# Performance work log

Hardware: AMD Instinct MI355X
Metric: run time of the kernel (lower is better)

Reference implementation:

```python
import jax, jax.numpy as jnp
import numpy as np

B, T, H = 32, 8192, 128

def setup_inputs() -> dict:
    key = jax.random.key(0)
    k1, k2, k3, k4, k5, k6 = jax.random.split(key, 6)
    stdv = 1.0 / np.sqrt(H)
    return {
        "hidden": jax.random.normal(k1, (B, H), jnp.float32),
        "encoder_outputs": jax.random.normal(k2, (T, B, H), jnp.float32),
        "len_seq": jax.random.randint(k3, (B,), 1, T + 1),  # valid lengths in [1, T]
        "W_attn": jax.random.normal(k4, (H, 2 * H), jnp.float32) * stdv,
        "b_attn": jnp.zeros((H,), jnp.float32),
        "v": jax.random.uniform(k5, (H,), jnp.float32, -stdv, stdv),
    }

def reference(hidden, encoder_outputs, len_seq, W_attn, b_attn, v):
    # hidden: [B,H]; encoder_outputs: [T,B,H]; len_seq: [B]
    T_ = encoder_outputs.shape[0]
    enc = jnp.transpose(encoder_outputs, (1, 0, 2))          # [B,T,H]
    h = jnp.broadcast_to(hidden[:, None, :], enc.shape)       # [B,T,H]
    # score(): relu(Linear(cat)) then v . energy
    energy = jax.nn.relu(jnp.concatenate([h, enc], axis=-1) @ W_attn.T + b_attn)  # [B,T,H]
    scores = jnp.einsum('bth,h->bt', energy, v)               # [B,T]
    # ragged masked softmax: softmax over first len_seq[i] positions, zeros after
    mask = jnp.arange(T_)[None, :] < len_seq[:, None]         # [B,T]
    attn = jax.nn.softmax(jnp.where(mask, scores, -jnp.inf), axis=1)
    attn = jnp.where(mask, attn, 0.0)
    return attn[:, None, :]                                   # [B,1,T]
```

## Files before the change

kernel.cpp:

```cpp
#include <hip/hip_runtime.h>
#include <hip/hip_bf16.h>

#define B 32
#define T 8192
#define H 128

typedef __attribute__((ext_vector_type(8)))  short short8_t;
typedef __attribute__((ext_vector_type(16))) float f32x16;

static __device__ __forceinline__ unsigned fbits(float x) { return __builtin_bit_cast(unsigned, x); }
static __device__ __forceinline__ float bfloat(unsigned u) { return __builtin_bit_cast(float, u); }

static __device__ __forceinline__ void pack4hi(const float4 f,
                                               unsigned& hi0, unsigned& hi1) {
    const unsigned u0 = fbits(f.x), u1 = fbits(f.y), u2 = fbits(f.z), u3 = fbits(f.w);
    hi0 = (u0 >> 16) | (u1 & 0xffff0000u);
    hi1 = (u2 >> 16) | (u3 & 0xffff0000u);
}

#define WPK_OFF  16384
#define PART_OFF 81920

__global__ void k_prep(const float* __restrict__ hidden,
                       const float* __restrict__ W_attn,
                       const float* __restrict__ b_attn,
                       float* __restrict__ u,
                       unsigned short* __restrict__ wpk) {
    const int tid = threadIdx.x;
    if (blockIdx.x < 32) {
        const int b = blockIdx.x;
        __shared__ float hrow[H];
        if (tid < H) hrow[tid] = hidden[b * H + tid];
        __syncthreads();
        if (tid < H) {
            const float* w = W_attn + (size_t)tid * (2 * H);
            float acc = b_attn[tid];
#pragma unroll
            for (int k = 0; k < H; ++k) acc = fmaf(w[k], hrow[k], acc);
            u[b * H + tid] = acc;
        }
    } else {
        const int idx  = (blockIdx.x - 32) * 256 + tid;
        const int s    = idx >> 8;
        const int m    = (idx >> 6) & 3;
        const int lane = idx & 63;
        const int h    = m * 32 + (lane & 31);
        const int k0   = s * 16 + (lane >> 5) * 8;
        const float* src = W_attn + (size_t)h * (2 * H) + H + k0;
        const int base = ((s * 4 + m) * 64 + lane) * 8;
#pragma unroll
        for (int e = 0; e < 8; ++e) {
            const float x = src[e];
            const unsigned ux = fbits(x);
            const unsigned hb = ux & 0xffff0000u;
            const float r = x - bfloat(hb);
            wpk[base + e]         = (unsigned short)(ux >> 16);
            wpk[16384 + base + e] = (unsigned short)(fbits(r) >> 16);
        }
    }
}

__global__ __launch_bounds__(512, 2) void k_scores_mfma(
    const float* __restrict__ enc,
    const float* __restrict__ u,
    const float* __restrict__ v,
    const unsigned short* __restrict__ wpk,
    const int* __restrict__ len_seq,
    float* __restrict__ scores,
    float* __restrict__ part)
{
    __shared__ uint2 hb[2][2048];
    __shared__ float cbuf[2][2][4][32];
    __shared__ float pm[2][32], ps[2][32];

    const int tid   = threadIdx.x;
    const int lane  = tid & 63;
    const int wid   = tid >> 6;
    const int tsel  = wid >> 2;
    const int mtile = wid & 3;
    const int l31   = lane & 31;
    const int kh    = lane >> 5;

    const int srow = tid >> 3;
    const int st8  = tid & 7;

    const int blk = blockIdx.x;
    const float4* enc4 = (const float4*)enc;

    const int lenrow = len_seq[srow & 31];
    const int tsb    = 2 * blk + (srow >> 5);

    short8_t w2hi[8], w2lo[8];
#pragma unroll
    for (int s = 0; s < 8; ++s) {
        const int fo = ((s * 4 + mtile) * 64 + lane) * 8;
        w2hi[s] = *(const short8_t*)(wpk + fo);
        w2lo[s] = *(const short8_t*)(wpk + 16384 + fo);
    }
    float4 uf[4], vv[4];
#pragma unroll
    for (int r4 = 0; r4 < 4; ++r4) {
        uf[r4] = *(const float4*)(u + l31 * H + mtile * 32 + r4 * 8 + kh * 4);
        vv[r4] = *(const float4*)(v + mtile * 32 + r4 * 8 + kh * 4);
    }
    const int lenb = len_seq[l31];

    float4 stg[4];
    {
        if (tsb < lenrow) {
            const float4* gs = enc4 + ((size_t)(2 * blk) * 32 + srow) * 32;
#pragma unroll
            for (int i = 0; i < 4; ++i) stg[i] = gs[st8 + 8 * i];
#pragma unroll
            for (int i = 0; i < 4; ++i) {
                unsigned hi0, hi1;
                pack4hi(stg[i], hi0, hi1);
                const int p16 = st8 + 8 * i;
                const int idx = srow * 32 + (((p16 >> 1) + srow) & 15) * 2 + (p16 & 1);
                hb[0][idx] = make_uint2(hi0, hi1);
            }
        }
        if (tsb + 512 < lenrow) {
            const float4* gs1 = enc4 + ((size_t)(2 * (blk + 256)) * 32 + srow) * 32;
#pragma unroll
            for (int i = 0; i < 4; ++i) stg[i] = gs1[st8 + 8 * i];
        }
    }
    __syncthreads();

    const int rrow  = tsel * 32 + l31;
    const int rbase = rrow * 32;

    float m_run = -1e30f, s_run = 0.0f;

#pragma unroll 1
    for (int q = 0; q < 16; ++q) {
        const int cur = q & 1, nxt = cur ^ 1;

        if (q < 15 && tsb + 512 * (q + 1) < lenrow) {
#pragma unroll
            for (int i = 0; i < 4; ++i) {
                unsigned hi0, hi1;
                pack4hi(stg[i], hi0, hi1);
                const int p16 = st8 + 8 * i;
                const int idx = srow * 32 + (((p16 >> 1) + srow) & 15) * 2 + (p16 & 1);
                hb[nxt][idx] = make_uint2(hi0, hi1);
            }
        }
        if (q < 14 && tsb + 512 * (q + 2) < lenrow) {
            const float4* gs = enc4 + ((size_t)(2 * (blk + 256 * (q + 2))) * 32 + srow) * 32;
#pragma unroll
            for (int i = 0; i < 4; ++i) stg[i] = gs[st8 + 8 * i];
        }

        f32x16 acc;
#pragma unroll
        for (int r4 = 0; r4 < 4; ++r4) {
            acc[4 * r4 + 0] = uf[r4].x; acc[4 * r4 + 1] = uf[r4].y;
            acc[4 * r4 + 2] = uf[r4].z; acc[4 * r4 + 3] = uf[r4].w;
        }

#pragma unroll
        for (int s = 0; s < 8; ++s) {
            const int slot = (2 * s + kh + l31) & 15;
            const short8_t bh = *(const short8_t*)&hb[cur][rbase + slot * 2];
            acc = __builtin_amdgcn_mfma_f32_32x32x16_bf16(w2hi[s], bh, acc, 0, 0, 0);
            acc = __builtin_amdgcn_mfma_f32_32x32x16_bf16(w2lo[s], bh, acc, 0, 0, 0);
        }

        float psum = 0.f;
#pragma unroll
        for (int r4 = 0; r4 < 4; ++r4) {
            psum = fmaf(fmaxf(acc[4 * r4 + 0], 0.f), vv[r4].x, psum);
            psum = fmaf(fmaxf(acc[4 * r4 + 1], 0.f), vv[r4].y, psum);
            psum = fmaf(fmaxf(acc[4 * r4 + 2], 0.f), vv[r4].z, psum);
            psum = fmaf(fmaxf(acc[4 * r4 + 3], 0.f), vv[r4].w, psum);
        }
        psum += __shfl_xor(psum, 32);

        if (lane < 32) cbuf[cur][tsel][mtile][l31] = psum;

        __syncthreads();

        if (mtile == 0 && lane < 32) {
            const float r = cbuf[cur][tsel][0][l31] + cbuf[cur][tsel][1][l31]
                          + cbuf[cur][tsel][2][l31] + cbuf[cur][tsel][3][l31];
            const int t = 2 * (blk + 256 * q) + tsel;
            scores[(size_t)l31 * T + t] = r;
            if (t < lenb) {
                const float m_new = fmaxf(m_run, r);
                s_run = s_run * __expf(m_run - m_new) + __expf(r - m_new);
                m_run = m_new;
            }
        }
    }

    if (mtile == 0 && lane < 32) { pm[tsel][l31] = m_run; ps[tsel][l31] = s_run; }
    __syncthreads();
    if (tid < 32) {
        const float m0 = pm[0][tid], m1 = pm[1][tid];
        const float s0 = ps[0][tid], s1 = ps[1][tid];
        const float M = fmaxf(m0, m1);
        const float S = s0 * __expf(m0 - M) + s1 * __expf(m1 - M);
        *(float2*)&part[((size_t)tid * 256 + blk) * 2] = make_float2(M, S);
    }
}

__global__ __launch_bounds__(256) void k_sm_final(
    float* __restrict__ out,
    const int* __restrict__ len_seq,
    const float* __restrict__ part)
{
    const int b    = blockIdx.x >> 3;
    const int c    = blockIdx.x & 7;
    const int tid  = threadIdx.x;
    const int lane = tid & 63;
    const int wid  = tid >> 6;
    const int len  = len_seq[b];

    __shared__ float rm[4], rs[4];

    float2 p = *(const float2*)&part[((size_t)b * 256 + tid) * 2];
    float m = p.x, s = p.y;
#pragma unroll
    for (int off = 32; off >= 1; off >>= 1) {
        const float m2 = __shfl_xor(m, off);
        const float s2 = __shfl_xor(s, off);
        const float M = fmaxf(m, m2);
        s = s * __expf(m - M) + s2 * __expf(m2 - M);
        m = M;
    }
    if (lane == 0) { rm[wid] = m; rs[wid] = s; }
    __syncthreads();
    const float M = fmaxf(fmaxf(rm[0], rm[1]), fmaxf(rm[2], rm[3]));
    const float S = rs[0] * __expf(rm[0] - M) + rs[1] * __expf(rm[1] - M)
                  + rs[2] * __expf(rm[2] - M) + rs[3] * __expf(rm[3] - M);
    const float inv = 1.0f / S;

    float* srow = out + (size_t)b * T + c * 1024;
#pragma unroll
    for (int i = 0; i < 4; ++i) {
        const int tl = tid + i * 256;
        const int t  = c * 1024 + tl;
        const float x = srow[tl];
        srow[tl] = (t < len) ? __expf(x - M) * inv : 0.0f;
    }
}

extern "C" void kernel_launch(void* const* d_in, const int* in_sizes, int n_in,
                              void* d_out, int out_size, void* d_ws, size_t ws_size,
                              hipStream_t stream) {
    const float* hidden = (const float*)d_in[0];
    const float* enc    = (const float*)d_in[1];
    const int*   len    = (const int*)d_in[2];
    const float* W      = (const float*)d_in[3];
    const float* bb     = (const float*)d_in[4];
    const float* v      = (const float*)d_in[5];

    float* out  = (float*)d_out;
    float* u_ws = (float*)d_ws;
    unsigned short* wpk = (unsigned short*)((char*)d_ws + WPK_OFF);
    float* part = (float*)((char*)d_ws + PART_OFF);

    k_prep<<<40, 256, 0, stream>>>(hidden, W, bb, u_ws, wpk);
    k_scores_mfma<<<256, 512, 0, stream>>>(enc, u_ws, v, wpk, len, out, part);
    k_sm_final<<<B * 8, 256, 0, stream>>>(out, len, part);
}
```

Measured before the change: 34.58 us.

## Fuse weight packing and hidden projection into scores kernel, drop prep launch

Removes the separate prep kernel and instead has each block of the scores kernel read W_attn directly, split it into bf16 hi/lo fragments in registers, and compute the hidden projection (u = W1·h + b) with split-bf16 MFMAs. This eliminates one kernel launch and the workspace round-trip for u and packed weights. In exchange, every block redundantly recomputes the projection and packing, adding prologue latency and register pressure, and the projection now uses a three-term bf16 split rather than full fp32 FMA.

```diff
diff --git a/kernel.cpp b/kernel.cpp
--- a/kernel.cpp
+++ b/kernel.cpp
@@ -10,6 +10,19 @@
 
 static __device__ __forceinline__ unsigned fbits(float x) { return __builtin_bit_cast(unsigned, x); }
 static __device__ __forceinline__ float bfloat(unsigned u) { return __builtin_bit_cast(float, u); }
+
+static __device__ __forceinline__ void pack4(const float4 f,
+                                             unsigned& hi0, unsigned& hi1,
+                                             unsigned& lo0, unsigned& lo1) {
+    const unsigned u0 = fbits(f.x), u1 = fbits(f.y), u2 = fbits(f.z), u3 = fbits(f.w);
+    const unsigned h0 = u0 & 0xffff0000u, h1 = u1 & 0xffff0000u;
+    const unsigned h2 = u2 & 0xffff0000u, h3 = u3 & 0xffff0000u;
+    const float r0 = f.x - bfloat(h0), r1 = f.y - bfloat(h1);
+    const float r2 = f.z - bfloat(h2), r3 = f.w - bfloat(h3);
+    hi0 = (u0 >> 16) | h1;                      hi1 = (u2 >> 16) | h3;
+    lo0 = (fbits(r0) >> 16) | (fbits(r1) & 0xffff0000u);
+    lo1 = (fbits(r2) >> 16) | (fbits(r3) & 0xffff0000u);
+}
 
 static __device__ __forceinline__ void pack4hi(const float4 f,
                                                unsigned& hi0, unsigned& hi1) {
@@ -18,53 +31,23 @@
     hi1 = (u2 >> 16) | (u3 & 0xffff0000u);
 }
 
-#define WPK_OFF  16384
+static __device__ __forceinline__ void pack_frag(const float4 a, const float4 b,
+                                                 short8_t& hi, short8_t& lo) {
+    union { short8_t v8; unsigned w[4]; } ph, pl;
+    unsigned h0, h1, l0, l1;
+    pack4(a, h0, h1, l0, l1); ph.w[0] = h0; ph.w[1] = h1; pl.w[0] = l0; pl.w[1] = l1;
+    pack4(b, h0, h1, l0, l1); ph.w[2] = h0; ph.w[3] = h1; pl.w[2] = l0; pl.w[3] = l1;
+    hi = ph.v8; lo = pl.v8;
+}
+
 #define PART_OFF 81920
-
-__global__ void k_prep(const float* __restrict__ hidden,
-                       const float* __restrict__ W_attn,
-                       const float* __restrict__ b_attn,
-                       float* __restrict__ u,
-                       unsigned short* __restrict__ wpk) {
-    const int tid = threadIdx.x;
-    if (blockIdx.x < 32) {
-        const int b = blockIdx.x;
-        __shared__ float hrow[H];
-        if (tid < H) hrow[tid] = hidden[b * H + tid];
-        __syncthreads();
-        if (tid < H) {
-            const float* w = W_attn + (size_t)tid * (2 * H);
-            float acc = b_attn[tid];
-#pragma unroll
-            for (int k = 0; k < H; ++k) acc = fmaf(w[k], hrow[k], acc);
-            u[b * H + tid] = acc;
-        }
-    } else {
-        const int idx  = (blockIdx.x - 32) * 256 + tid;
-        const int s    = idx >> 8;
-        const int m    = (idx >> 6) & 3;
-        const int lane = idx & 63;
-        const int h    = m * 32 + (lane & 31);
-        const int k0   = s * 16 + (lane >> 5) * 8;
-        const float* src = W_attn + (size_t)h * (2 * H) + H + k0;
-        const int base = ((s * 4 + m) * 64 + lane) * 8;
-#pragma unroll
-        for (int e = 0; e < 8; ++e) {
-            const float x = src[e];
-            const unsigned ux = fbits(x);
-            const unsigned hb = ux & 0xffff0000u;
-            const float r = x - bfloat(hb);
-            wpk[base + e]         = (unsigned short)(ux >> 16);
-            wpk[16384 + base + e] = (unsigned short)(fbits(r) >> 16);
-        }
-    }
-}
 
 __global__ __launch_bounds__(512, 2) void k_scores_mfma(
     const float* __restrict__ enc,
-    const float* __restrict__ u,
+    const float* __restrict__ hidden,
+    const float* __restrict__ b_attn,
+    const float* __restrict__ W_attn,
     const float* __restrict__ v,
-    const unsigned short* __restrict__ wpk,
     const int* __restrict__ len_seq,
     float* __restrict__ scores,
     float* __restrict__ part)
@@ -91,18 +74,45 @@
     const int tsb    = 2 * blk + (srow >> 5);
 
     short8_t w2hi[8], w2lo[8];
-#pragma unroll
-    for (int s = 0; s < 8; ++s) {
-        const int fo = ((s * 4 + mtile) * 64 + lane) * 8;
-        w2hi[s] = *(const short8_t*)(wpk + fo);
-        w2lo[s] = *(const short8_t*)(wpk + 16384 + fo);
-    }
-    float4 uf[4], vv[4];
-#pragma unroll
-    for (int r4 = 0; r4 < 4; ++r4) {
-        uf[r4] = *(const float4*)(u + l31 * H + mtile * 32 + r4 * 8 + kh * 4);
+    {
+        const int h = mtile * 32 + l31;
+        const float* wrow = W_attn + (size_t)h * (2 * H) + H;
+#pragma unroll
+        for (int s = 0; s < 8; ++s) {
+            const int k0 = s * 16 + kh * 8;
+            const float4 a = *(const float4*)(wrow + k0);
+            const float4 b = *(const float4*)(wrow + k0 + 4);
+            pack_frag(a, b, w2hi[s], w2lo[s]);
+        }
+    }
+
+    f32x16 uacc;
+    {
+#pragma unroll
+        for (int r4 = 0; r4 < 4; ++r4) {
+            const float4 bb4 = *(const float4*)(b_attn + mtile * 32 + r4 * 8 + kh * 4);
+            uacc[4 * r4 + 0] = bb4.x; uacc[4 * r4 + 1] = bb4.y;
+            uacc[4 * r4 + 2] = bb4.z; uacc[4 * r4 + 3] = bb4.w;
+        }
+        const int h = mtile * 32 + l31;
+        const float* wrow = W_attn + (size_t)h * (2 * H);
+        const float* xrow = hidden + l31 * H;
+#pragma unroll
+        for (int s = 0; s < 8; ++s) {
+            const int k0 = s * 16 + kh * 8;
+            short8_t w1h, w1l, xh, xl;
+            pack_frag(*(const float4*)(wrow + k0), *(const float4*)(wrow + k0 + 4), w1h, w1l);
+            pack_frag(*(const float4*)(xrow + k0), *(const float4*)(xrow + k0 + 4), xh, xl);
+            uacc = __builtin_amdgcn_mfma_f32_32x32x16_bf16(w1h, xh, uacc, 0, 0, 0);
+            uacc = __builtin_amdgcn_mfma_f32_32x32x16_bf16(w1l, xh, uacc, 0, 0, 0);
+            uacc = __builtin_amdgcn_mfma_f32_32x32x16_bf16(w1h, xl, uacc, 0, 0, 0);
+        }
+    }
+
+    float4 vv[4];
+#pragma unroll
+    for (int r4 = 0; r4 < 4; ++r4)
         vv[r4] = *(const float4*)(v + mtile * 32 + r4 * 8 + kh * 4);
-    }
     const int lenb = len_seq[l31];
 
     float4 stg[4];
@@ -153,12 +163,7 @@
             for (int i = 0; i < 4; ++i) stg[i] = gs[st8 + 8 * i];
         }
 
-        f32x16 acc;
-#pragma unroll
-        for (int r4 = 0; r4 < 4; ++r4) {
-            acc[4 * r4 + 0] = uf[r4].x; acc[4 * r4 + 1] = uf[r4].y;
-            acc[4 * r4 + 2] = uf[r4].z; acc[4 * r4 + 3] = uf[r4].w;
-        }
+        f32x16 acc = uacc;
 
 #pragma unroll
         for (int s = 0; s < 8; ++s) {
@@ -258,11 +263,8 @@
     const float* v      = (const float*)d_in[5];
 
     float* out  = (float*)d_out;
-    float* u_ws = (float*)d_ws;
-    unsigned short* wpk = (unsigned short*)((char*)d_ws + WPK_OFF);
     float* part = (float*)((char*)d_ws + PART_OFF);
 
-    k_prep<<<40, 256, 0, stream>>>(hidden, W, bb, u_ws, wpk);
-    k_scores_mfma<<<256, 512, 0, stream>>>(enc, u_ws, v, wpk, len, out, part);
+    k_scores_mfma<<<256, 512, 0, stream>>>(enc, hidden, bb, W, v, len, out, part);
     k_sm_final<<<B * 8, 256, 0, stream>>>(out, len, part);
 }
```

Result: slower. 39.56 us (+14.4%).

## Process four timesteps per iteration to halve loop trips and barriers

Applied to the files above, without the earlier changes.

Each block iteration now covers four timesteps instead of two. Each wave runs two MFMA tiles per iteration, and the staging loads double to eight float4 per thread. This halves the number of loop iterations and __syncthreads barriers and gives more memory traffic in flight per thread. In exchange it doubles LDS use and raises register pressure from the larger staging buffer, which may hurt occupancy under launch_bounds(512,2).

```diff
diff --git a/kernel.cpp b/kernel.cpp
--- a/kernel.cpp
+++ b/kernel.cpp
@@ -69,8 +69,8 @@
     float* __restrict__ scores,
     float* __restrict__ part)
 {
-    __shared__ uint2 hb[2][2048];
-    __shared__ float cbuf[2][2][4][32];
+    __shared__ uint2 hb[2][4096];
+    __shared__ float cbuf[2][4][4][32];
     __shared__ float pm[2][32], ps[2][32];
 
     const int tid   = threadIdx.x;
@@ -81,14 +81,14 @@
     const int l31   = lane & 31;
     const int kh    = lane >> 5;
 
-    const int srow = tid >> 3;
-    const int st8  = tid & 7;
+    const int srow = tid >> 2;
+    const int st4  = tid & 3;
 
     const int blk = blockIdx.x;
     const float4* enc4 = (const float4*)enc;
 
     const int lenrow = len_seq[srow & 31];
-    const int tsb    = 2 * blk + (srow >> 5);
+    const int tsb    = 4 * blk + (srow >> 5);
 
     short8_t w2hi[8], w2lo[8];
 #pragma unroll
@@ -105,92 +105,99 @@
     }
     const int lenb = len_seq[l31];
 
-    float4 stg[4];
+    float4 stg[8];
     {
         if (tsb < lenrow) {
-            const float4* gs = enc4 + ((size_t)(2 * blk) * 32 + srow) * 32;
-#pragma unroll
-            for (int i = 0; i < 4; ++i) stg[i] = gs[st8 + 8 * i];
-#pragma unroll
-            for (int i = 0; i < 4; ++i) {
+            const float4* gs = enc4 + ((size_t)(4 * blk) * 32 + srow) * 32;
+#pragma unroll
+            for (int i = 0; i < 8; ++i) stg[i] = gs[st4 + 4 * i];
+#pragma unroll
+            for (int i = 0; i < 8; ++i) {
                 unsigned hi0, hi1;
                 pack4hi(stg[i], hi0, hi1);
-                const int p16 = st8 + 8 * i;
+                const int p16 = st4 + 4 * i;
                 const int idx = srow * 32 + (((p16 >> 1) + srow) & 15) * 2 + (p16 & 1);
                 hb[0][idx] = make_uint2(hi0, hi1);
             }
         }
-        if (tsb + 512 < lenrow) {
-            const float4* gs1 = enc4 + ((size_t)(2 * (blk + 256)) * 32 + srow) * 32;
-#pragma unroll
-            for (int i = 0; i < 4; ++i) stg[i] = gs1[st8 + 8 * i];
+        if (tsb + 1024 < lenrow) {
+            const float4* gs1 = enc4 + ((size_t)(4 * (blk + 256)) * 32 + srow) * 32;
+#pragma unroll
+            for (int i = 0; i < 8; ++i) stg[i] = gs1[st4 + 4 * i];
         }
     }
     __syncthreads();
 
-    const int rrow  = tsel * 32 + l31;
-    const int rbase = rrow * 32;
-
     float m_run = -1e30f, s_run = 0.0f;
 
 #pragma unroll 1
-    for (int q = 0; q < 16; ++q) {
+    for (int q = 0; q < 8; ++q) {
         const int cur = q & 1, nxt = cur ^ 1;
 
-        if (q < 15 && tsb + 512 * (q + 1) < lenrow) {
-#pragma unroll
-            for (int i = 0; i < 4; ++i) {
+        if (q < 7 && tsb + 1024 * (q + 1) < lenrow) {
+#pragma unroll
+            for (int i = 0; i < 8; ++i) {
                 unsigned hi0, hi1;
                 pack4hi(stg[i], hi0, hi1);
-                const int p16 = st8 + 8 * i;
+                const int p16 = st4 + 4 * i;
                 const int idx = srow * 32 + (((p16 >> 1) + srow) & 15) * 2 + (p16 & 1);
                 hb[nxt][idx] = make_uint2(hi0, hi1);
             }
         }
-        if (q < 14 && tsb + 512 * (q + 2) < lenrow) {
-            const float4* gs = enc4 + ((size_t)(2 * (blk + 256 * (q + 2))) * 32 + srow) * 32;
-#pragma unroll
-            for (int i = 0; i < 4; ++i) stg[i] = gs[st8 + 8 * i];
-        }
-
-        f32x16 acc;
-#pragma unroll
-        for (int r4 = 0; r4 < 4; ++r4) {
-            acc[4 * r4 + 0] = uf[r4].x; acc[4 * r4 + 1] = uf[r4].y;
-            acc[4 * r4 + 2] = uf[r4].z; acc[4 * r4 + 3] = uf[r4].w;
-        }
-
-#pragma unroll
-        for (int s = 0; s < 8; ++s) {
-            const int slot = (2 * s + kh + l31) & 15;
-            const short8_t bh = *(const short8_t*)&hb[cur][rbase + slot * 2];
-            acc = __builtin_amdgcn_mfma_f32_32x32x16_bf16(w2hi[s], bh, acc, 0, 0, 0);
-            acc = __builtin_amdgcn_mfma_f32_32x32x16_bf16(w2lo[s], bh, acc, 0, 0, 0);
-        }
-
-        float psum = 0.f;
-#pragma unroll
-        for (int r4 = 0; r4 < 4; ++r4) {
-            psum = fmaf(fmaxf(acc[4 * r4 + 0], 0.f), vv[r4].x, psum);
-            psum = fmaf(fmaxf(acc[4 * r4 + 1], 0.f), vv[r4].y, psum);
-            psum = fmaf(fmaxf(acc[4 * r4 + 2], 0.f), vv[r4].z, psum);
-            psum = fmaf(fmaxf(acc[4 * r4 + 3], 0.f), vv[r4].w, psum);
-        }
-        psum += __shfl_xor(psum, 32);
-
-        if (lane < 32) cbuf[cur][tsel][mtile][l31] = psum;
+        if (q < 6 && tsb + 1024 * (q + 2) < lenrow) {
+            const float4* gs = enc4 + ((size_t)(4 * (blk + 256 * (q + 2))) * 32 + srow) * 32;
+#pragma unroll
+            for (int i = 0; i < 8; ++i) stg[i] = gs[st4 + 4 * i];
+        }
+
+#pragma unroll
+        for (int tt = 0; tt < 2; ++tt) {
+            const int tloc  = 2 * tsel + tt;
+            const int rbase = (tloc * 32 + l31) * 32;
+
+            f32x16 acc;
+#pragma unroll
+            for (int r4 = 0; r4 < 4; ++r4) {
+                acc[4 * r4 + 0] = uf[r4].x; acc[4 * r4 + 1] = uf[r4].y;
+                acc[4 * r4 + 2] = uf[r4].z; acc[4 * r4 + 3] = uf[r4].w;
+            }
+
+#pragma unroll
+            for (int s = 0; s < 8; ++s) {
+                const int slot = (2 * s + kh + l31) & 15;
+                const short8_t bh = *(const short8_t*)&hb[cur][rbase + slot * 2];
+                acc = __builtin_amdgcn_mfma_f32_32x32x16_bf16(w2hi[s], bh, acc, 0, 0, 0);
+                acc = __builtin_amdgcn_mfma_f32_32x32x16_bf16(w2lo[s], bh, acc, 0, 0, 0);
+            }
+
+            float psum = 0.f;
+#pragma unroll
+            for (int r4 = 0; r4 < 4; ++r4) {
+                psum = fmaf(fmaxf(acc[4 * r4 + 0], 0.f), vv[r4].x, psum);
+                psum = fmaf(fmaxf(acc[4 * r4 + 1], 0.f), vv[r4].y, psum);
+                psum = fmaf(fmaxf(acc[4 * r4 + 2], 0.f), vv[r4].z, psum);
+                psum = fmaf(fmaxf(acc[4 * r4 + 3], 0.f), vv[r4].w, psum);
+            }
+            psum += __shfl_xor(psum, 32);
+
+            if (lane < 32) cbuf[cur][tloc][mtile][l31] = psum;
+        }
 
         __syncthreads();
 
         if (mtile == 0 && lane < 32) {
-            const float r = cbuf[cur][tsel][0][l31] + cbuf[cur][tsel][1][l31]
-                          + cbuf[cur][tsel][2][l31] + cbuf[cur][tsel][3][l31];
-            const int t = 2 * (blk + 256 * q) + tsel;
-            scores[(size_t)l31 * T + t] = r;
-            if (t < lenb) {
-                const float m_new = fmaxf(m_run, r);
-                s_run = s_run * __expf(m_run - m_new) + __expf(r - m_new);
-                m_run = m_new;
+#pragma unroll
+            for (int tt = 0; tt < 2; ++tt) {
+                const int tloc = 2 * tsel + tt;
+                const float r = cbuf[cur][tloc][0][l31] + cbuf[cur][tloc][1][l31]
+                              + cbuf[cur][tloc][2][l31] + cbuf[cur][tloc][3][l31];
+                const int t = 4 * (blk + 256 * q) + tloc;
+                scores[(size_t)l31 * T + t] = r;
+                if (t < lenb) {
+                    const float m_new = fmaxf(m_run, r);
+                    s_run = s_run * __expf(m_run - m_new) + __expf(r - m_new);
+                    m_run = m_new;
+                }
             }
         }
     }
```

Measured after the change: 38.57 us. +11.5%, slower.
